# Performance work log

Hardware: AMD Instinct MI355X
Metric: run time of the kernel (lower is better)

The kernel has to match this reference:

```python
import jax, jax.numpy as jnp
import numpy as np

EPS = 1e-5


def _bn_eval(h, mean, var, gamma, beta):
    # BatchNorm1d in eval mode: normalize with running stats, then affine.
    return (h - mean) * (gamma / jnp.sqrt(var + EPS)) + beta


def setup_inputs() -> dict:
    key = jax.random.key(0)
    ks = jax.random.split(key, 17)
    B, D_IN, N_HEADS = 1024, 200, 128
    s = lambda k, shape, scale: jax.random.normal(k, shape, dtype=jnp.float32) * scale
    return {
        "x": s(ks[0], (B, D_IN), 1.0),
        # shared trunk
        "W0": s(ks[1], (D_IN, 2048), 1.0 / np.sqrt(D_IN)),
        "b0": s(ks[2], (2048,), 0.01),
        "g0": jax.random.uniform(ks[3], (2048,), dtype=jnp.float32, minval=0.5, maxval=1.5),
        "be0": s(ks[4], (2048,), 0.01),
        "m0": s(ks[5], (2048,), 0.1),
        "v0": jax.random.uniform(ks[6], (2048,), dtype=jnp.float32, minval=0.5, maxval=1.5),
        "W1": s(ks[7], (2048, 1024), 1.0 / np.sqrt(2048)),
        "b1": s(ks[8], (1024,), 0.01),
        "g1": jax.random.uniform(ks[9], (1024,), dtype=jnp.float32, minval=0.5, maxval=1.5),
        "be1": s(ks[10], (1024,), 0.01),
        "m1": s(ks[11], (1024,), 0.1),
        "v1": jax.random.uniform(ks[12], (1024,), dtype=jnp.float32, minval=0.5, maxval=1.5),
        # 128 parallel byte-predictor heads, stacked on axis 0
        "HW1": s(ks[13], (N_HEADS, 1024, 512), 1.0 / np.sqrt(1024)),
        "Hb1": s(ks[14], (N_HEADS, 512), 0.01),
        "HW2": s(ks[15], (N_HEADS, 512, 256), 1.0 / np.sqrt(512)),
        "Hb2": s(ks[16], (N_HEADS, 256), 0.01),
    }


def reference(x, W0, b0, g0, be0, m0, v0, W1, b1, g1, be1, m1, v1, HW1, Hb1, HW2, Hb2):
    # shared trunk: Linear -> BN -> ReLU -> (Dropout=id) -> Linear -> BN -> ReLU
    h = jax.nn.relu(_bn_eval(x @ W0 + b0, m0, v0, g0, be0))            # [B, 2048]
    feats = jax.nn.relu(_bn_eval(h @ W1 + b1, m1, v1, g1, be1))         # [B, 1024]
    # all 128 heads in one batched GEMM pair (equivalent to the per-head loop)
    z = jax.nn.relu(jnp.einsum('bd,ndh->bnh', feats, HW1) + Hb1)        # [B, 128, 512]
    out = jnp.einsum('bnh,nho->bno', z, HW2) + Hb2                      # [B, 128, 256]
    return out
```

## Files before the change

### kernel.cpp

```cpp
#include <hip/hip_runtime.h>
#include <hip/hip_bf16.h>
#include <stdint.h>


typedef __bf16 bf16x8 __attribute__((ext_vector_type(8)));
typedef float  floatx4 __attribute__((ext_vector_type(4)));
typedef unsigned short ushortx4 __attribute__((ext_vector_type(4)));
typedef unsigned short ushortx8 __attribute__((ext_vector_type(8)));

typedef __attribute__((address_space(1))) void as1_void;
typedef __attribute__((address_space(3))) void as3_void;

__device__ __forceinline__ void gld_lds16(const void* g, void* l) {
    __builtin_amdgcn_global_load_lds((as1_void*)g, (as3_void*)l, 16, 0, 0);
}

__device__ __forceinline__ unsigned short f2bf(float f) {
    __hip_bfloat16 h = __float2bfloat16(f);
    unsigned short s;
    __builtin_memcpy(&s, &h, 2);
    return s;
}

template <int MODE, typename OutT>
__global__ __launch_bounds__(256, 2)
void gemm_bt(const short* __restrict__ A, int lda, long aBatch,
             const short* __restrict__ B, int ldb, long bBatch,
             OutT* __restrict__ C, int ldc, long cBatch,
             int K, int ntilesN,
             const float* __restrict__ p0, const float* __restrict__ p1,
             const float* __restrict__ p2, const float* __restrict__ p3,
             const float* __restrict__ p4, int pBatch)
{
    __shared__ short As[128 * 32];
    __shared__ short Bs[128 * 32];

    const int tid  = threadIdx.x;
    const int w    = tid >> 6;
    const int l    = tid & 63;
    const int head = blockIdx.y;
    const int mt   = blockIdx.x / ntilesN;
    const int nt   = blockIdx.x % ntilesN;
    const int m0   = mt * 128;
    const int n0   = nt * 128;

    A += (long)head * aBatch;
    B += (long)head * bBatch;
    C += (long)head * cBatch;
    const float* pb = p0 + (long)head * pBatch;

    const int wm   = (w >> 1) * 64;
    const int wn   = (w & 1) * 64;
    const int lrow = l & 15;
    const int lk   = (l >> 4) * 8;

    floatx4 acc[4][4] = {};

    const int srow = l >> 2;
    const int scol = (l & 3) * 8;
    const short* Ag = A + (long)(m0 + w * 16 + srow) * lda + scol;
    const short* Bg = B + (long)(n0 + w * 16 + srow) * ldb + scol;
    const long a64 = (long)64 * lda;
    const long b64 = (long)64 * ldb;
    short* AsW0 = &As[(w * 16) * 32];
    short* AsW1 = &As[(64 + w * 16) * 32];
    short* BsW0 = &Bs[(w * 16) * 32];
    short* BsW1 = &Bs[(64 + w * 16) * 32];

    for (int k0 = 0; k0 < K; k0 += 32) {
        gld_lds16(Ag + k0,       AsW0);
        gld_lds16(Ag + a64 + k0, AsW1);
        gld_lds16(Bg + k0,       BsW0);
        gld_lds16(Bg + b64 + k0, BsW1);
        __syncthreads();

        bf16x8 af[4], bfr[4];
#pragma unroll
        for (int i = 0; i < 4; ++i)
            af[i] = *(const bf16x8*)&As[(wm + i * 16 + lrow) * 32 + lk];
#pragma unroll
        for (int j = 0; j < 4; ++j)
            bfr[j] = *(const bf16x8*)&Bs[(wn + j * 16 + lrow) * 32 + lk];

#pragma unroll
        for (int i = 0; i < 4; ++i)
#pragma unroll
            for (int j = 0; j < 4; ++j)
                acc[i][j] = __builtin_amdgcn_mfma_f32_16x16x32_bf16(
                    af[i], bfr[j], acc[i][j], 0, 0, 0);
        __syncthreads();
    }

    const int erow = (l >> 4) * 4;
    const int ecol = l & 15;
#pragma unroll
    for (int j = 0; j < 4; ++j) {
        const int nj = n0 + wn + j * 16 + ecol;
        float scale = 1.f, shift;
        if constexpr (MODE == 0) {
            const float s = p1[nj] * rsqrtf(p4[nj] + 1e-5f);
            scale = s;
            shift = (pb[nj] - p3[nj]) * s + p2[nj];
        } else {
            shift = pb[nj];
        }
#pragma unroll
        for (int i = 0; i < 4; ++i) {
            const long mi = m0 + wm + i * 16 + erow;
#pragma unroll
            for (int r = 0; r < 4; ++r) {
                float v = acc[i][j][r] * scale + shift;
                if constexpr (MODE != 2) v = fmaxf(v, 0.f);
                const long idx = (mi + r) * (long)ldc + nj;
                if constexpr (sizeof(OutT) == 2) C[idx] = (OutT)f2bf(v);
                else                             C[idx] = (OutT)v;
            }
        }
    }
}

__global__ __launch_bounds__(256)
void transpose64(const float* __restrict__ in, unsigned short* __restrict__ out,
                 int R, int C, long inBatch, long outBatch)
{
    __shared__ unsigned short lt[64 * 68];
    in  += (long)blockIdx.z * inBatch;
    out += (long)blockIdx.z * outBatch;
    const int c0 = blockIdx.x * 64;
    const int r0 = blockIdx.y * 64;
    const int t  = threadIdx.x;

    {
        const int rb = t >> 4;
        const int cg = (t & 15) * 4;
        floatx4 v[4];
#pragma unroll
        for (int i = 0; i < 4; ++i)
            v[i] = *(const floatx4*)&in[(long)(r0 + rb * 4 + i) * C + c0 + cg];
#pragma unroll
        for (int j = 0; j < 4; ++j) {
            ushortx4 col;
#pragma unroll
            for (int i = 0; i < 4; ++i) col[i] = f2bf(v[i][j]);
            *(ushortx4*)&lt[(cg + j) * 68 + rb * 4] = col;
        }
    }
    __syncthreads();

#pragma unroll
    for (int it = 0; it < 2; ++it) {
        const int idx = t + it * 256;
        const int c   = idx >> 3;
        const int rc  = idx & 7;
        ushortx4 lo = *(const ushortx4*)&lt[c * 68 + rc * 8];
        ushortx4 hi = *(const ushortx4*)&lt[c * 68 + rc * 8 + 4];
        ushortx8 o;
        o[0] = lo[0]; o[1] = lo[1]; o[2] = lo[2]; o[3] = lo[3];
        o[4] = hi[0]; o[5] = hi[1]; o[6] = hi[2]; o[7] = hi[3];
        *(ushortx8*)&out[(long)(c0 + c) * R + r0 + rc * 8] = o;
    }
}

__global__ void transpose_f32_bf16(const float* __restrict__ in, short* __restrict__ out,
                                   int R, int C, int Rpad, long inBatch, long outBatch)
{
    __shared__ float tile[32][33];
    in  += (long)blockIdx.z * inBatch;
    out += (long)blockIdx.z * outBatch;
    const int c0 = blockIdx.x * 32;
    const int r0 = blockIdx.y * 32;
    const int tx = threadIdx.x, ty = threadIdx.y;
#pragma unroll
    for (int rr = 0; rr < 4; ++rr) {
        const int r = r0 + ty + rr * 8;
        float v = 0.f;
        if (r < R) v = in[(long)r * C + c0 + tx];
        tile[ty + rr * 8][tx] = v;
    }
    __syncthreads();
#pragma unroll
    for (int rr = 0; rr < 4; ++rr) {
        const int oc = ty + rr * 8;
        out[(long)(c0 + oc) * Rpad + r0 + tx] = (short)f2bf(tile[tx][oc]);
    }
}

__global__ void pad_convert(const float* __restrict__ in, short* __restrict__ out,
                            int C, int Cpad, int total)
{
    const int idx = blockIdx.x * 256 + threadIdx.x;
    if (idx >= total) return;
    const int r = idx / Cpad, c = idx % Cpad;
    out[idx] = (short)f2bf(c < C ? in[(long)r * C + c] : 0.f);
}


extern "C" void kernel_launch(void* const* d_in, const int* in_sizes, int n_in,
                              void* d_out, int out_size, void* d_ws, size_t ws_size,
                              hipStream_t stream)
{
    const float* x   = (const float*)d_in[0];
    const float* W0  = (const float*)d_in[1];
    const float* b0  = (const float*)d_in[2];
    const float* g0  = (const float*)d_in[3];
    const float* be0 = (const float*)d_in[4];
    const float* m0  = (const float*)d_in[5];
    const float* v0  = (const float*)d_in[6];
    const float* W1  = (const float*)d_in[7];
    const float* b1  = (const float*)d_in[8];
    const float* g1  = (const float*)d_in[9];
    const float* be1 = (const float*)d_in[10];
    const float* m1  = (const float*)d_in[11];
    const float* v1  = (const float*)d_in[12];
    const float* HW1 = (const float*)d_in[13];
    const float* Hb1 = (const float*)d_in[14];
    const float* HW2 = (const float*)d_in[15];
    const float* Hb2 = (const float*)d_in[16];
    float* out = (float*)d_out;

    char* ws = (char*)d_ws;
    size_t off = 0;
    short* xb   = (short*)(ws + off); off += (size_t)1024 * 224 * 2;
    short* W0T  = (short*)(ws + off); off += (size_t)2048 * 224 * 2;
    short* W1T  = (short*)(ws + off); off += (size_t)1024 * 2048 * 2;
    short* HW1T = (short*)(ws + off); off += (size_t)128 * 512 * 1024 * 2;
    short* HW2T = (short*)(ws + off); off += (size_t)128 * 256 * 512 * 2;
    short* h    = (short*)(ws + off); off += (size_t)1024 * 2048 * 2;
    short* fts  = (short*)(ws + off); off += (size_t)1024 * 1024 * 2;
    short* z    = (short*)(ws + off); off += (size_t)1024 * 128 * 512 * 2;

    pad_convert<<<dim3((1024 * 224) / 256), dim3(256), 0, stream>>>(x, xb, 200, 224, 1024 * 224);
    transpose_f32_bf16<<<dim3(64, 7, 1), dim3(32, 8), 0, stream>>>(W0, W0T, 200, 2048, 224, 0, 0);
    transpose64<<<dim3(16, 32, 1), dim3(256), 0, stream>>>(
        W1, (unsigned short*)W1T, 2048, 1024, 0, 0);
    transpose64<<<dim3(8, 16, 128), dim3(256), 0, stream>>>(
        HW1, (unsigned short*)HW1T, 1024, 512, (long)1024 * 512, (long)512 * 1024);
    transpose64<<<dim3(4, 8, 128), dim3(256), 0, stream>>>(
        HW2, (unsigned short*)HW2T, 512, 256, (long)512 * 256, (long)256 * 512);

    gemm_bt<0, short><<<dim3(8 * 16, 1), dim3(256), 0, stream>>>(
        xb, 224, 0, W0T, 224, 0, h, 2048, 0, 224, 16, b0, g0, be0, m0, v0, 0);
    gemm_bt<0, short><<<dim3(8 * 8, 1), dim3(256), 0, stream>>>(
        h, 2048, 0, W1T, 2048, 0, fts, 1024, 0, 2048, 8, b1, g1, be1, m1, v1, 0);
    gemm_bt<1, short><<<dim3(8 * 4, 128), dim3(256), 0, stream>>>(
        fts, 1024, 0, HW1T, 1024, (long)512 * 1024, z, 128 * 512, 512,
        1024, 4, Hb1, nullptr, nullptr, nullptr, nullptr, 512);
    gemm_bt<2, float><<<dim3(8 * 2, 128), dim3(256), 0, stream>>>(
        z, 128 * 512, 512, HW2T, 512, (long)256 * 512, out, 128 * 256, 256,
        512, 2, Hb2, nullptr, nullptr, nullptr, nullptr, 256);

    (void)in_sizes; (void)n_in; (void)out_size; (void)ws_size;
}
```

Before: 811.8 us.

## Add 256x256-tile 8-wave GEMM with interleaved LDS staging for head GEMMs

Adds a new gemm8 kernel with 256x256 output tiles, 512 threads (8 waves), double-buffered LDS loaded through global_load_lds, and MFMA phases interleaved with staging of the next K tiles under s_setprio. The block index is swizzled so neighbouring tiles go to different XCDs. The two per-head GEMMs now use this kernel, which dominate runtime. The aim is higher data reuse per tile and better overlap of loads with MFMA. In exchange it needs 128KB of LDS and many accumulator registers, which limits occupancy, and the hand-placed waitcnt/barrier schedule is fragile.

```diff
diff --git a/kernel.cpp b/kernel.cpp
--- a/kernel.cpp
+++ b/kernel.cpp
@@ -111,6 +111,202 @@
             for (int r = 0; r < 4; ++r) {
                 float v = acc[i][j][r] * scale + shift;
                 if constexpr (MODE != 2) v = fmaxf(v, 0.f);
+                const long idx = (mi + r) * (long)ldc + nj;
+                if constexpr (sizeof(OutT) == 2) C[idx] = (OutT)f2bf(v);
+                else                             C[idx] = (OutT)v;
+            }
+        }
+    }
+}
+
+template <int MODE, typename OutT>
+__global__ __launch_bounds__(512, 2)
+void gemm8(const short* __restrict__ A, int lda, long aBatch,
+           const short* __restrict__ B, int ldb, long bBatch,
+           OutT* __restrict__ C, int ldc, long cBatch,
+           int K, int ntilesN, int tilesPerHead,
+           const float* __restrict__ bias, int pBatch)
+{
+    __shared__ __attribute__((aligned(128))) char lds[131072];
+
+    const int tid = threadIdx.x;
+    const int w   = tid >> 6;
+    const int l   = tid & 63;
+    const int wm  = w >> 2;
+    const int wn  = w & 3;
+
+    const int nwg  = gridDim.x;
+    const int cpx  = nwg >> 3;
+    const int bid  = blockIdx.x;
+    const int swz  = (bid & 7) * cpx + (bid >> 3);
+    const int head = swz / tilesPerHead;
+    const int tile = swz - head * tilesPerHead;
+    const int mt   = tile / ntilesN;
+    const int nt   = tile - mt * ntilesN;
+    const int m0   = mt * 256;
+    const int n0   = nt * 256;
+
+    const short* Ag = A + (long)head * aBatch + (long)m0 * lda;
+    const short* Bg = B + (long)head * bBatch + (long)n0 * ldb;
+    C += (long)head * cBatch;
+    const float* pb = bias + (long)head * pBatch;
+
+    int rowL[2], k0L[2];
+#pragma unroll
+    for (int li = 0; li < 2; ++li) {
+        const int i  = tid + li * 512;
+        const int id = i >> 6;
+        const int j  = i & 63;
+        const int jo = j ^ (((j >> 5) & 1) << 1);
+        rowL[li] = (id >> 1) * 16 + (jo >> 2);
+        k0L[li]  = (id & 1) * 32 + (jo & 3) * 8;
+    }
+    const int ldsW = w * 1024;
+
+    const int lrow    = l & 15;
+    const int fragoff = (lrow * 64 + (l >> 4) * 16) ^ (((lrow >> 3) & 1) << 5);
+
+    const int nkt = K >> 6;
+
+#define STAGE(srcbase, ld_, kt_, h_, region)                                     \
+    do {                                                                         \
+        gld_lds16((srcbase) + (long)((h_) * 128 + rowL[0]) * (ld_) +             \
+                      (kt_) * 64 + k0L[0],                                       \
+                  (region) + (h_) * 16384 + ldsW);                               \
+        gld_lds16((srcbase) + (long)((h_) * 128 + rowL[1]) * (ld_) +             \
+                      (kt_) * 64 + k0L[1],                                       \
+                  (region) + (h_) * 16384 + ldsW + 8192);                        \
+    } while (0)
+
+    char* const ldsA0 = lds;
+    char* const ldsB0 = lds + 65536;
+
+    STAGE(Ag, lda, 0, 0, ldsA0);
+    STAGE(Ag, lda, 0, 1, ldsA0);
+    STAGE(Bg, ldb, 0, 0, ldsB0);
+    STAGE(Bg, ldb, 0, 1, ldsB0);
+    if (nkt > 1) {
+        STAGE(Bg, ldb, 1, 0, ldsB0 + 32768);
+        STAGE(Bg, ldb, 1, 1, ldsB0 + 32768);
+        asm volatile("s_waitcnt vmcnt(4)" ::: "memory");
+    } else {
+        asm volatile("s_waitcnt vmcnt(0)" ::: "memory");
+    }
+    __builtin_amdgcn_sched_barrier(0);
+    __builtin_amdgcn_s_barrier();
+
+    floatx4 acc[8][4] = {};
+    bf16x8 a[4][2], b[4][2];
+    const int aSr = wm * 8;
+    const int bSr = wn * 4;
+
+    for (int kt = 0; kt < nkt; ++kt) {
+        char* const ldsA  = ldsA0 + (kt & 1) * 32768;
+        char* const ldsB  = ldsB0 + (kt & 1) * 32768;
+        char* const ldsAn = ldsA0 + ((kt & 1) ^ 1) * 32768;
+
+#pragma unroll
+        for (int m = 0; m < 4; ++m) {
+            a[m][0] = *(const bf16x8*)(ldsA + ((aSr + m) * 2 + 0) * 1024 + fragoff);
+            a[m][1] = *(const bf16x8*)(ldsA + ((aSr + m) * 2 + 1) * 1024 + fragoff);
+        }
+#pragma unroll
+        for (int n = 0; n < 2; ++n) {
+            b[n][0] = *(const bf16x8*)(ldsB + ((bSr + n) * 2 + 0) * 1024 + fragoff);
+            b[n][1] = *(const bf16x8*)(ldsB + ((bSr + n) * 2 + 1) * 1024 + fragoff);
+        }
+        if (kt + 1 < nkt) { STAGE(Ag, lda, kt + 1, 0, ldsAn); }
+        __builtin_amdgcn_s_barrier();
+        asm volatile("s_waitcnt lgkmcnt(0)" ::: "memory");
+        __builtin_amdgcn_sched_barrier(0);
+        __builtin_amdgcn_s_setprio(1);
+#pragma unroll
+        for (int m = 0; m < 4; ++m)
+#pragma unroll
+            for (int n = 0; n < 2; ++n)
+#pragma unroll
+                for (int ks = 0; ks < 2; ++ks)
+                    acc[m][n] = __builtin_amdgcn_mfma_f32_16x16x32_bf16(
+                        a[m][ks], b[n][ks], acc[m][n], 0, 0, 0);
+        __builtin_amdgcn_s_setprio(0);
+        __builtin_amdgcn_s_barrier();
+
+#pragma unroll
+        for (int n = 2; n < 4; ++n) {
+            b[n][0] = *(const bf16x8*)(ldsB + ((bSr + n) * 2 + 0) * 1024 + fragoff);
+            b[n][1] = *(const bf16x8*)(ldsB + ((bSr + n) * 2 + 1) * 1024 + fragoff);
+        }
+        if (kt + 1 < nkt) { STAGE(Ag, lda, kt + 1, 1, ldsAn); }
+        __builtin_amdgcn_s_barrier();
+        asm volatile("s_waitcnt lgkmcnt(0)" ::: "memory");
+        __builtin_amdgcn_sched_barrier(0);
+        __builtin_amdgcn_s_setprio(1);
+#pragma unroll
+        for (int m = 0; m < 4; ++m)
+#pragma unroll
+            for (int n = 2; n < 4; ++n)
+#pragma unroll
+                for (int ks = 0; ks < 2; ++ks)
+                    acc[m][n] = __builtin_amdgcn_mfma_f32_16x16x32_bf16(
+                        a[m][ks], b[n][ks], acc[m][n], 0, 0, 0);
+        __builtin_amdgcn_s_setprio(0);
+        __builtin_amdgcn_s_barrier();
+
+#pragma unroll
+        for (int m = 0; m < 4; ++m) {
+            a[m][0] = *(const bf16x8*)(ldsA + ((aSr + 4 + m) * 2 + 0) * 1024 + fragoff);
+            a[m][1] = *(const bf16x8*)(ldsA + ((aSr + 4 + m) * 2 + 1) * 1024 + fragoff);
+        }
+        if (kt + 2 < nkt) { STAGE(Bg, ldb, kt + 2, 0, ldsB); }
+        __builtin_amdgcn_s_barrier();
+        asm volatile("s_waitcnt lgkmcnt(0)" ::: "memory");
+        __builtin_amdgcn_sched_barrier(0);
+        __builtin_amdgcn_s_setprio(1);
+#pragma unroll
+        for (int m = 0; m < 4; ++m)
+#pragma unroll
+            for (int n = 2; n < 4; ++n)
+#pragma unroll
+                for (int ks = 0; ks < 2; ++ks)
+                    acc[m + 4][n] = __builtin_amdgcn_mfma_f32_16x16x32_bf16(
+                        a[m][ks], b[n][ks], acc[m + 4][n], 0, 0, 0);
+        __builtin_amdgcn_s_setprio(0);
+        __builtin_amdgcn_s_barrier();
+
+        if (kt + 2 < nkt) { STAGE(Bg, ldb, kt + 2, 1, ldsB); }
+        __builtin_amdgcn_s_setprio(1);
+#pragma unroll
+        for (int m = 0; m < 4; ++m)
+#pragma unroll
+            for (int n = 0; n < 2; ++n)
+#pragma unroll
+                for (int ks = 0; ks < 2; ++ks)
+                    acc[m + 4][n] = __builtin_amdgcn_mfma_f32_16x16x32_bf16(
+                        a[m][ks], b[n][ks], acc[m + 4][n], 0, 0, 0);
+        __builtin_amdgcn_s_setprio(0);
+        if (kt + 2 < nkt) {
+            asm volatile("s_waitcnt vmcnt(4)" ::: "memory");
+        } else if (kt + 1 < nkt) {
+            asm volatile("s_waitcnt vmcnt(0)" ::: "memory");
+        }
+        __builtin_amdgcn_sched_barrier(0);
+        __builtin_amdgcn_s_barrier();
+    }
+#undef STAGE
+
+    const int erow = (l >> 4) * 4;
+    const int ecol = l & 15;
+#pragma unroll
+    for (int n = 0; n < 4; ++n) {
+        const int nj = n0 + wn * 64 + n * 16 + ecol;
+        const float shift = pb[nj];
+#pragma unroll
+        for (int m = 0; m < 8; ++m) {
+            const long mi = m0 + wm * 128 + m * 16 + erow;
+#pragma unroll
+            for (int r = 0; r < 4; ++r) {
+                float v = acc[m][n][r] + shift;
+                if constexpr (MODE == 1) v = fmaxf(v, 0.f);
                 const long idx = (mi + r) * (long)ldc + nj;
                 if constexpr (sizeof(OutT) == 2) C[idx] = (OutT)f2bf(v);
                 else                             C[idx] = (OutT)v;
@@ -242,12 +438,12 @@
         xb, 224, 0, W0T, 224, 0, h, 2048, 0, 224, 16, b0, g0, be0, m0, v0, 0);
     gemm_bt<0, short><<<dim3(8 * 8, 1), dim3(256), 0, stream>>>(
         h, 2048, 0, W1T, 2048, 0, fts, 1024, 0, 2048, 8, b1, g1, be1, m1, v1, 0);
-    gemm_bt<1, short><<<dim3(8 * 4, 128), dim3(256), 0, stream>>>(
+    gemm8<1, short><<<dim3(8 * 128), dim3(512), 0, stream>>>(
         fts, 1024, 0, HW1T, 1024, (long)512 * 1024, z, 128 * 512, 512,
-        1024, 4, Hb1, nullptr, nullptr, nullptr, nullptr, 512);
-    gemm_bt<2, float><<<dim3(8 * 2, 128), dim3(256), 0, stream>>>(
+        1024, 2, 8, Hb1, 512);
+    gemm8<2, float><<<dim3(4 * 128), dim3(512), 0, stream>>>(
         z, 128 * 512, 512, HW2T, 512, (long)256 * 512, out, 128 * 256, 256,
-        512, 2, Hb2, nullptr, nullptr, nullptr, nullptr, 256);
+        512, 1, 4, Hb2, 256);
 
     (void)in_sizes; (void)n_in; (void)out_size; (void)ws_size;
 }
```

New measurement: 780.8 us. 3.8% less time.
